# Performance work log

Hardware: AMD Instinct MI355X
Metric: run time of the kernel (lower is better)

## Reference

```python
import jax, jax.numpy as jnp
import numpy as np

N = 200_000   # nodes
E = 6_400_000 # edges (avg degree 32)


def setup_inputs() -> dict:
    key = jax.random.key(0)
    k = jax.random.split(key, 6)
    x = jax.random.normal(k[0], (N, 2), dtype=jnp.float32)
    edge_index = jax.random.randint(k[1], (2, E), 0, N, dtype=jnp.int32)
    # GCNConv(2, 8) and GCNConv(8, 4) parameters (Glorot-ish init, zero bias as in PyG)
    W1 = jax.random.normal(k[2], (2, 8), dtype=jnp.float32) * (1.0 / np.sqrt(2.0))
    b1 = jnp.zeros((8,), dtype=jnp.float32)
    W2 = jax.random.normal(k[3], (8, 4), dtype=jnp.float32) * (1.0 / np.sqrt(8.0))
    b2 = jnp.zeros((4,), dtype=jnp.float32)
    return {"x": x, "edge_index": edge_index, "W1": W1, "b1": b1, "W2": W2, "b2": b2}


def _gcn_conv(x, src, dst, norm, W, b, n):
    # PyG GCNConv: linear transform, normalized gather/scatter-add, bias after aggregation
    h = x @ W                                   # [N, F_out]
    msg = h[src] * norm[:, None]                # gather + edge-wise scale, [E', F_out]
    agg = jax.ops.segment_sum(msg, dst, num_segments=n)  # scatter-add at targets
    return agg + b


def reference(x, edge_index, W1, b1, W2, b2):
    n = x.shape[0]
    # add self-loops (PyG default add_self_loops=True)
    loops = jnp.arange(n, dtype=edge_index.dtype)
    src = jnp.concatenate([edge_index[0], loops])
    dst = jnp.concatenate([edge_index[1], loops])
    # symmetric degree normalization: deg computed at targets with unit edge weights
    deg = jax.ops.segment_sum(jnp.ones_like(src, dtype=x.dtype), dst, num_segments=n)
    deg_inv_sqrt = jnp.where(deg > 0, jax.lax.rsqrt(jnp.maximum(deg, 1.0)), 0.0)
    norm = deg_inv_sqrt[src] * deg_inv_sqrt[dst]  # [E']

    h = jax.nn.relu(_gcn_conv(x, src, dst, norm, W1, b1, n))
    out = _gcn_conv(h, src, dst, norm, W2, b2, n)
    return out
```

## Files before the change

### kernel.cpp

```cpp
#include <hip/hip_runtime.h>


#define EPB   8192
#define PART  2048
#define LPBIT 11
#define SRCB  18
#define BC    4
#define RSTR  2049
#define STCAP 17408


__global__ __launch_bounds__(512) void countA_kernel(
    const int* __restrict__ dst, int* __restrict__ cntmat, int E, int P) {
    __shared__ int cnt[128];
    int tid = threadIdx.x;
    if (tid < 128) cnt[tid] = 0;
    __syncthreads();
    int nv4 = E >> 2;
    int b4 = (blockIdx.x * EPB) >> 2;
    int e4 = min(b4 + (EPB >> 2), nv4);
    const int4* d4 = (const int4*)dst;
    #pragma unroll
    for (int k = 0; k < (EPB >> 2); k += 512) {
        int i = b4 + k + tid;
        if (i < e4) {
            int4 d = d4[i];
            atomicAdd(&cnt[d.x >> LPBIT], 1);
            atomicAdd(&cnt[d.y >> LPBIT], 1);
            atomicAdd(&cnt[d.z >> LPBIT], 1);
            atomicAdd(&cnt[d.w >> LPBIT], 1);
        }
    }
    if (blockIdx.x == gridDim.x - 1) {
        int e = (nv4 << 2) + tid;
        if (e < E) atomicAdd(&cnt[dst[e] >> LPBIT], 1);
    }
    __syncthreads();
    int* row = cntmat + (size_t)blockIdx.x * P;
    if (tid < P) row[tid] = cnt[tid];
}

__global__ __launch_bounds__(256) void colscanA_kernel(
    int* __restrict__ cntmat, int* __restrict__ colTotal, int B, int P) {
    __shared__ int sdata[256];
    int p = blockIdx.x, tid = threadIdx.x;
    int v[4];
    int s = 0;
    #pragma unroll
    for (int k = 0; k < 4; k++) {
        int b = tid * 4 + k;
        v[k] = (b < B) ? cntmat[(size_t)b * P + p] : 0;
        s += v[k];
    }
    int x = s;
    sdata[tid] = x;
    __syncthreads();
    for (int off = 1; off < 256; off <<= 1) {
        int t = (tid >= off) ? sdata[tid - off] : 0;
        __syncthreads();
        x += t;
        sdata[tid] = x;
        __syncthreads();
    }
    int run = x - s;
    #pragma unroll
    for (int k = 0; k < 4; k++) {
        int b = tid * 4 + k;
        if (b < B) cntmat[(size_t)b * P + p] = run;
        run += v[k];
    }
    if (tid == 255) colTotal[p] = x;
}

__global__ __launch_bounds__(256) void totalscanA_kernel(
    const int* __restrict__ colTotal, int* __restrict__ colStart,
    int P, int E) {
    __shared__ int sdata[256];
    int tid = threadIdx.x;
    int v[4];
    int s = 0;
    #pragma unroll
    for (int k = 0; k < 4; k++) {
        int i = tid * 4 + k;
        v[k] = (i < P) ? colTotal[i] : 0;
        s += v[k];
    }
    int x = s;
    sdata[tid] = x;
    __syncthreads();
    for (int off = 1; off < 256; off <<= 1) {
        int t = (tid >= off) ? sdata[tid - off] : 0;
        __syncthreads();
        x += t;
        sdata[tid] = x;
        __syncthreads();
    }
    int run = x - s;
    #pragma unroll
    for (int k = 0; k < 4; k++) {
        int i = tid * 4 + k;
        if (i < P) colStart[i] = run;
        run += v[k];
    }
    if (tid == 0) colStart[P] = E;
}

__global__ __launch_bounds__(512) void scatterA_kernel(
    const int* __restrict__ src, const int* __restrict__ dst,
    const int* __restrict__ cntmat, const int* __restrict__ colStart,
    unsigned* __restrict__ packed, int E, int P) {
    __shared__ int cur[128];
    int tid = threadIdx.x;
    if (tid < P) cur[tid] = colStart[tid] + cntmat[(size_t)blockIdx.x * P + tid];
    __syncthreads();
    int nv4 = E >> 2;
    int b4 = (blockIdx.x * EPB) >> 2;
    int e4 = min(b4 + (EPB >> 2), nv4);
    const int4* d4 = (const int4*)dst;
    const int4* s4 = (const int4*)src;
    #pragma unroll
    for (int k = 0; k < (EPB >> 2); k += 512) {
        int i = b4 + k + tid;
        if (i < e4) {
            int4 d = d4[i];
            int4 sv = s4[i];
            int p0 = atomicAdd(&cur[d.x >> LPBIT], 1);
            packed[p0] = ((unsigned)(d.x & (PART - 1)) << SRCB) | (unsigned)sv.x;
            int p1 = atomicAdd(&cur[d.y >> LPBIT], 1);
            packed[p1] = ((unsigned)(d.y & (PART - 1)) << SRCB) | (unsigned)sv.y;
            int p2 = atomicAdd(&cur[d.z >> LPBIT], 1);
            packed[p2] = ((unsigned)(d.z & (PART - 1)) << SRCB) | (unsigned)sv.z;
            int p3 = atomicAdd(&cur[d.w >> LPBIT], 1);
            packed[p3] = ((unsigned)(d.w & (PART - 1)) << SRCB) | (unsigned)sv.w;
        }
    }
    if (blockIdx.x == gridDim.x - 1) {
        int e = (nv4 << 2) + tid;
        if (e < E) {
            int d = dst[e];
            int pos = atomicAdd(&cur[d >> LPBIT], 1);
            packed[pos] = ((unsigned)(d & (PART - 1)) << SRCB) | (unsigned)src[e];
        }
    }
}


__global__ __launch_bounds__(512) void localC_kernel(
    const unsigned* __restrict__ packed, const int* __restrict__ colStart,
    int* __restrict__ runStart, int* __restrict__ srcsorted) {
    __shared__ int hist[PART];
    __shared__ int sdata[512];
    __shared__ unsigned stage[STCAP];
    int tid = threadIdx.x;
    int dp = blockIdx.x >> 2, b = blockIdx.x & (BC - 1);
    int s0 = colStart[dp], len = colStart[dp + 1] - s0;
    int lo = s0 + (int)(((long long)len * b) / BC);
    int hi = s0 + (int)(((long long)len * (b + 1)) / BC);
    for (int k = tid; k < PART; k += 512) hist[k] = 0;
    __syncthreads();
    for (int i = lo + tid; i < hi; i += 512)
        atomicAdd(&hist[packed[i] >> SRCB], 1);
    __syncthreads();
    int off = tid * 4;
    int v0 = hist[off], v1 = hist[off + 1], v2 = hist[off + 2], v3 = hist[off + 3];
    int s = v0 + v1 + v2 + v3;
    int x = s;
    sdata[tid] = x;
    __syncthreads();
    for (int o = 1; o < 512; o <<= 1) {
        int t = (tid >= o) ? sdata[tid - o] : 0;
        __syncthreads();
        x += t;
        sdata[tid] = x;
        __syncthreads();
    }
    int run = x - s;
    int* rs = runStart + (size_t)(dp * BC + b) * RSTR;
    int c0 = lo + run, c1 = c0 + v0, c2 = c1 + v1, c3 = c2 + v2;
    rs[off] = c0; rs[off + 1] = c1; rs[off + 2] = c2; rs[off + 3] = c3;
    __syncthreads();
    hist[off] = c0; hist[off + 1] = c1; hist[off + 2] = c2; hist[off + 3] = c3;
    if (tid == 0) rs[PART] = hi;
    __syncthreads();
    int total = hi - lo;
    bool ovf = total > STCAP;
    for (int i = lo + tid; i < hi; i += 512) {
        unsigned w = packed[i];
        int pos = atomicAdd(&hist[w >> SRCB], 1);
        unsigned sv = w & ((1u << SRCB) - 1);
        if (!ovf) stage[pos - lo] = sv;
        else srcsorted[pos] = sv;
    }
    __syncthreads();
    if (!ovf)
        for (int j = tid; j < total; j += 512) srcsorted[lo + j] = (int)stage[j];
}


__global__ __launch_bounds__(512) void dinvg_kernel(
    const int* __restrict__ runStart, const float* __restrict__ x,
    float* __restrict__ dinv, float* __restrict__ g, int n) {
    int i = blockIdx.x * 512 + threadIdx.x;
    if (i >= n) return;
    int dp = i >> LPBIT, ld = i & (PART - 1);
    int deg = 0;
    #pragma unroll
    for (int b = 0; b < BC; b++) {
        const int* rs = runStart + (size_t)(dp * BC + b) * RSTR + ld;
        deg += rs[1] - rs[0];
    }
    float d = rsqrtf((float)deg + 1.0f);
    dinv[i] = d;
    float2 xv = ((const float2*)x)[i];
    ((float2*)g)[i] = make_float2(xv.x * d, xv.y * d);
}

__global__ __launch_bounds__(512) void agg1_kernel(
    const int* __restrict__ runStart, const int* __restrict__ srcsorted,
    const float* __restrict__ g, const float* __restrict__ dinv,
    const float* __restrict__ W1, const float* __restrict__ b1,
    const float* __restrict__ W2, float* __restrict__ hs2, int n) {
    int i = blockIdx.x * 512 + threadIdx.x;
    if (i >= n) return;
    int dp = i >> LPBIT, ld = i & (PART - 1);
    const float2* gp = (const float2*)g;
    float s0 = 0.0f, s1 = 0.0f;
    #pragma unroll
    for (int b = 0; b < BC; b++) {
        const int* rs = runStart + (size_t)(dp * BC + b) * RSTR + ld;
        int p0 = rs[0], p1 = rs[1];
        int p = p0;
        for (; p + 4 <= p1; p += 4) {
            int a = srcsorted[p], bb = srcsorted[p + 1];
            int c = srcsorted[p + 2], e = srcsorted[p + 3];
            float2 w0 = gp[a], w1 = gp[bb], w2 = gp[c], w3 = gp[e];
            s0 += w0.x + w1.x + w2.x + w3.x;
            s1 += w0.y + w1.y + w2.y + w3.y;
        }
        for (; p < p1; p++) {
            float2 w = gp[srcsorted[p]];
            s0 += w.x;
            s1 += w.y;
        }
    }
    float d = dinv[i];
    float2 gi = gp[i];
    s0 = (s0 + gi.x) * d;
    s1 = (s1 + gi.y) * d;
    float h[8];
    #pragma unroll
    for (int f = 0; f < 8; f++)
        h[f] = fmaxf(s0 * W1[f] + s1 * W1[8 + f] + b1[f], 0.0f);
    float oc[4];
    #pragma unroll
    for (int k = 0; k < 4; k++) {
        float a = 0.0f;
        #pragma unroll
        for (int f = 0; f < 8; f++) a += h[f] * W2[4 * f + k];
        oc[k] = a * d;
    }
    float4 o;
    o.x = oc[0]; o.y = oc[1]; o.z = oc[2]; o.w = oc[3];
    *(float4*)(hs2 + 4 * (size_t)i) = o;
}

__global__ __launch_bounds__(512) void agg2_kernel(
    const int* __restrict__ runStart, const int* __restrict__ srcsorted,
    const float* __restrict__ hs2, const float* __restrict__ dinv,
    const float* __restrict__ b2, float* __restrict__ out, int n) {
    int i = blockIdx.x * 512 + threadIdx.x;
    if (i >= n) return;
    int dp = i >> LPBIT, ld = i & (PART - 1);
    const float4* hp = (const float4*)hs2;
    float s0 = 0.0f, s1 = 0.0f, s2 = 0.0f, s3 = 0.0f;
    #pragma unroll
    for (int b = 0; b < BC; b++) {
        const int* rs = runStart + (size_t)(dp * BC + b) * RSTR + ld;
        int p0 = rs[0], p1 = rs[1];
        int p = p0;
        for (; p + 4 <= p1; p += 4) {
            int a = srcsorted[p], bb = srcsorted[p + 1];
            int c = srcsorted[p + 2], e = srcsorted[p + 3];
            float4 w0 = hp[a], w1 = hp[bb], w2 = hp[c], w3 = hp[e];
            s0 += w0.x + w1.x + w2.x + w3.x;
            s1 += w0.y + w1.y + w2.y + w3.y;
            s2 += w0.z + w1.z + w2.z + w3.z;
            s3 += w0.w + w1.w + w2.w + w3.w;
        }
        for (; p < p1; p++) {
            float4 w = hp[srcsorted[p]];
            s0 += w.x; s1 += w.y; s2 += w.z; s3 += w.w;
        }
    }
    float d = dinv[i];
    float4 hi2 = hp[i];
    float4 o;
    o.x = d * (s0 + hi2.x) + b2[0];
    o.y = d * (s1 + hi2.y) + b2[1];
    o.z = d * (s2 + hi2.z) + b2[2];
    o.w = d * (s3 + hi2.w) + b2[3];
    *(float4*)(out + 4 * (size_t)i) = o;
}

extern "C" void kernel_launch(void* const* d_in, const int* in_sizes, int n_in,
                              void* d_out, int out_size, void* d_ws, size_t ws_size,
                              hipStream_t stream) {
    const float* x   = (const float*)d_in[0];
    const int*   ei  = (const int*)d_in[1];
    const float* W1  = (const float*)d_in[2];
    const float* b1  = (const float*)d_in[3];
    const float* W2  = (const float*)d_in[4];
    const float* b2  = (const float*)d_in[5];
    float* out = (float*)d_out;

    const int n = in_sizes[0] / 2;
    const int E = in_sizes[1] / 2;
    const int* src = ei;
    const int* dst = ei + E;

    const int P  = (n + PART - 1) >> LPBIT;
    const int B1 = (E + EPB - 1) / EPB;

    int* ws = (int*)d_ws;
    int* colTotal = ws;
    int* colStart = ws + 1024;
    int* cntmatA  = ws + 2048;
    size_t cmsz = (((size_t)B1 * P) + 3) & ~(size_t)3;
    int* runStart = cntmatA + cmsz;
    size_t rssz = (((size_t)P * BC * RSTR) + 3) & ~(size_t)3;
    unsigned* packed = (unsigned*)(runStart + rssz);
    int* srcsorted = (int*)(packed + E);
    size_t nd = (size_t)P << LPBIT;
    float* dinv = (float*)packed;
    float* g    = dinv + nd;
    float* hs2  = g + 2 * nd;

    const int gN = (n + 511) / 512;

    countA_kernel    <<<B1, 512, 0, stream>>>(dst, cntmatA, E, P);
    colscanA_kernel  <<<P, 256, 0, stream>>>(cntmatA, colTotal, B1, P);
    totalscanA_kernel<<<1, 256, 0, stream>>>(colTotal, colStart, P, E);
    scatterA_kernel  <<<B1, 512, 0, stream>>>(src, dst, cntmatA, colStart, packed, E, P);
    localC_kernel    <<<P * BC, 512, 0, stream>>>(packed, colStart, runStart, srcsorted);
    dinvg_kernel     <<<gN, 512, 0, stream>>>(runStart, x, dinv, g, n);
    agg1_kernel      <<<gN, 512, 0, stream>>>(runStart, srcsorted, g, dinv, W1, b1, W2, hs2, n);
    agg2_kernel      <<<gN, 512, 0, stream>>>(runStart, srcsorted, hs2, dinv, b2, out, n);
}
```

Measured before the change: 247.6 us.

## Stage gathered neighbor features in LDS and aggregate with per-slice partials

Each aggregation layer is split into a partial kernel and a combine kernel. In the partial kernel, a block owns a slice of destination nodes within one bucket, cooperatively gathers all neighbor feature rows into shared memory with coalesced index reads, and then sums per node per feature channel. A separate combine kernel adds the partials across the four buckets and applies the dense transforms. This is meant to replace the thread-per-node gather loops, which suffer load imbalance and divergence, at the cost of two extra launches and a partial buffer round trip through global memory.

```diff
diff --git a/kernel.cpp b/kernel.cpp
--- a/kernel.cpp
+++ b/kernel.cpp
@@ -8,6 +8,10 @@
 #define BC    4
 #define RSTR  2049
 #define STCAP 17408
+#define NSL1  256
+#define CAP1  2304
+#define NSL2  128
+#define CAP2  1280
 
 
 __global__ __launch_bounds__(512) void countA_kernel(
@@ -189,7 +193,7 @@
         int pos = atomicAdd(&hist[w >> SRCB], 1);
         unsigned sv = w & ((1u << SRCB) - 1);
         if (!ovf) stage[pos - lo] = sv;
-        else srcsorted[pos] = sv;
+        else srcsorted[pos] = (int)sv;
     }
     __syncthreads();
     if (!ovf)
@@ -215,91 +219,130 @@
     ((float2*)g)[i] = make_float2(xv.x * d, xv.y * d);
 }
 
-__global__ __launch_bounds__(512) void agg1_kernel(
-    const int* __restrict__ runStart, const int* __restrict__ srcsorted,
-    const float* __restrict__ g, const float* __restrict__ dinv,
-    const float* __restrict__ W1, const float* __restrict__ b1,
-    const float* __restrict__ W2, float* __restrict__ hs2, int n) {
+
+__global__ __launch_bounds__(512) void agg1p_kernel(
+    const int* __restrict__ srcsorted, const int* __restrict__ runStart,
+    const float* __restrict__ g, float* __restrict__ partial1) {
+    __shared__ float2 stage[CAP1];
+    __shared__ int srs[NSL1 + 1];
+    int tid = threadIdx.x;
+    int bid = blockIdx.x;
+    int sl = bid & 7, rb = bid >> 3;
+    const int* rs = runStart + (size_t)rb * RSTR + sl * NSL1;
+    if (tid <= NSL1) srs[tid] = rs[tid];
+    __syncthreads();
+    int lo = srs[0], hi = srs[NSL1];
+    const float2* gp = (const float2*)g;
+    bool ovf = (hi - lo) > CAP1;
+    if (!ovf)
+        for (int e = lo + tid; e < hi; e += 512)
+            stage[e - lo] = gp[srcsorted[e]];
+    __syncthreads();
+    int nid = tid >> 1, c = tid & 1;
+    int a = srs[nid] - lo, bnd = srs[nid + 1] - lo;
+    float acc = 0.0f;
+    if (!ovf) {
+        const float* st = (const float*)stage;
+        for (int j = a; j < bnd; j++) acc += st[j * 2 + c];
+    } else {
+        for (int j = a; j < bnd; j++)
+            acc += g[2 * (size_t)srcsorted[lo + j] + c];
+    }
+    partial1[(size_t)bid * 512 + tid] = acc;
+}
+
+__global__ __launch_bounds__(512) void combine1_kernel(
+    const float* __restrict__ partial1, const float* __restrict__ g,
+    const float* __restrict__ dinv, const float* __restrict__ W1,
+    const float* __restrict__ b1, const float* __restrict__ W2,
+    float* __restrict__ hs2, int n) {
     int i = blockIdx.x * 512 + threadIdx.x;
     if (i >= n) return;
     int dp = i >> LPBIT, ld = i & (PART - 1);
-    const float2* gp = (const float2*)g;
+    int sl = ld >> 8, off = ld & (NSL1 - 1);
     float s0 = 0.0f, s1 = 0.0f;
     #pragma unroll
     for (int b = 0; b < BC; b++) {
-        const int* rs = runStart + (size_t)(dp * BC + b) * RSTR + ld;
-        int p0 = rs[0], p1 = rs[1];
-        int p = p0;
-        for (; p + 4 <= p1; p += 4) {
-            int a = srcsorted[p], bb = srcsorted[p + 1];
-            int c = srcsorted[p + 2], e = srcsorted[p + 3];
-            float2 w0 = gp[a], w1 = gp[bb], w2 = gp[c], w3 = gp[e];
-            s0 += w0.x + w1.x + w2.x + w3.x;
-            s1 += w0.y + w1.y + w2.y + w3.y;
-        }
-        for (; p < p1; p++) {
-            float2 w = gp[srcsorted[p]];
-            s0 += w.x;
-            s1 += w.y;
-        }
+        int bid = ((dp * BC + b) << 3) | sl;
+        const float* q = partial1 + (size_t)bid * 512 + off * 2;
+        s0 += q[0];
+        s1 += q[1];
     }
     float d = dinv[i];
-    float2 gi = gp[i];
+    float2 gi = ((const float2*)g)[i];
     s0 = (s0 + gi.x) * d;
     s1 = (s1 + gi.y) * d;
-    float h[8];
-    #pragma unroll
-    for (int f = 0; f < 8; f++)
-        h[f] = fmaxf(s0 * W1[f] + s1 * W1[8 + f] + b1[f], 0.0f);
-    float oc[4];
-    #pragma unroll
-    for (int k = 0; k < 4; k++) {
-        float a = 0.0f;
-        #pragma unroll
-        for (int f = 0; f < 8; f++) a += h[f] * W2[4 * f + k];
-        oc[k] = a * d;
+    float oc0 = 0.0f, oc1 = 0.0f, oc2 = 0.0f, oc3 = 0.0f;
+    #pragma unroll
+    for (int f = 0; f < 8; f++) {
+        float h = fmaxf(s0 * W1[f] + s1 * W1[8 + f] + b1[f], 0.0f);
+        oc0 += h * W2[4 * f];
+        oc1 += h * W2[4 * f + 1];
+        oc2 += h * W2[4 * f + 2];
+        oc3 += h * W2[4 * f + 3];
     }
     float4 o;
-    o.x = oc[0]; o.y = oc[1]; o.z = oc[2]; o.w = oc[3];
-    *(float4*)(hs2 + 4 * (size_t)i) = o;
-}
-
-__global__ __launch_bounds__(512) void agg2_kernel(
-    const int* __restrict__ runStart, const int* __restrict__ srcsorted,
-    const float* __restrict__ hs2, const float* __restrict__ dinv,
-    const float* __restrict__ b2, float* __restrict__ out, int n) {
+    o.x = oc0 * d; o.y = oc1 * d; o.z = oc2 * d; o.w = oc3 * d;
+    ((float4*)hs2)[i] = o;
+}
+
+__global__ __launch_bounds__(512) void agg2p_kernel(
+    const int* __restrict__ srcsorted, const int* __restrict__ runStart,
+    const float* __restrict__ hs2, float* __restrict__ partial2) {
+    __shared__ float4 stage[CAP2];
+    __shared__ int srs[NSL2 + 1];
+    int tid = threadIdx.x;
+    int bid = blockIdx.x;
+    int sl = bid & 15, rb = bid >> 4;
+    const int* rs = runStart + (size_t)rb * RSTR + sl * NSL2;
+    if (tid <= NSL2) srs[tid] = rs[tid];
+    __syncthreads();
+    int lo = srs[0], hi = srs[NSL2];
+    const float4* hp = (const float4*)hs2;
+    bool ovf = (hi - lo) > CAP2;
+    if (!ovf)
+        for (int e = lo + tid; e < hi; e += 512)
+            stage[e - lo] = hp[srcsorted[e]];
+    __syncthreads();
+    int nid = tid >> 2, c = tid & 3;
+    int a = srs[nid] - lo, bnd = srs[nid + 1] - lo;
+    float acc = 0.0f;
+    if (!ovf) {
+        const float* st = (const float*)stage;
+        for (int j = a; j < bnd; j++) acc += st[j * 4 + c];
+    } else {
+        for (int j = a; j < bnd; j++)
+            acc += hs2[4 * (size_t)srcsorted[lo + j] + c];
+    }
+    partial2[(size_t)bid * 512 + tid] = acc;
+}
+
+__global__ __launch_bounds__(512) void combine2_kernel(
+    const float* __restrict__ partial2, const float* __restrict__ hs2,
+    const float* __restrict__ dinv, const float* __restrict__ b2,
+    float* __restrict__ out, int n) {
     int i = blockIdx.x * 512 + threadIdx.x;
     if (i >= n) return;
     int dp = i >> LPBIT, ld = i & (PART - 1);
-    const float4* hp = (const float4*)hs2;
+    int sl = ld >> 7, off = ld & (NSL2 - 1);
     float s0 = 0.0f, s1 = 0.0f, s2 = 0.0f, s3 = 0.0f;
     #pragma unroll
     for (int b = 0; b < BC; b++) {
-        const int* rs = runStart + (size_t)(dp * BC + b) * RSTR + ld;
-        int p0 = rs[0], p1 = rs[1];
-        int p = p0;
-        for (; p + 4 <= p1; p += 4) {
-            int a = srcsorted[p], bb = srcsorted[p + 1];
-            int c = srcsorted[p + 2], e = srcsorted[p + 3];
-            float4 w0 = hp[a], w1 = hp[bb], w2 = hp[c], w3 = hp[e];
-            s0 += w0.x + w1.x + w2.x + w3.x;
-            s1 += w0.y + w1.y + w2.y + w3.y;
-            s2 += w0.z + w1.z + w2.z + w3.z;
-            s3 += w0.w + w1.w + w2.w + w3.w;
-        }
-        for (; p < p1; p++) {
-            float4 w = hp[srcsorted[p]];
-            s0 += w.x; s1 += w.y; s2 += w.z; s3 += w.w;
-        }
+        int bid = ((dp * BC + b) << 4) | sl;
+        const float* q = partial2 + (size_t)bid * 512 + off * 4;
+        s0 += q[0];
+        s1 += q[1];
+        s2 += q[2];
+        s3 += q[3];
     }
     float d = dinv[i];
-    float4 hi2 = hp[i];
+    float4 hv = ((const float4*)hs2)[i];
     float4 o;
-    o.x = d * (s0 + hi2.x) + b2[0];
-    o.y = d * (s1 + hi2.y) + b2[1];
-    o.z = d * (s2 + hi2.z) + b2[2];
-    o.w = d * (s3 + hi2.w) + b2[3];
-    *(float4*)(out + 4 * (size_t)i) = o;
+    o.x = d * (s0 + hv.x) + b2[0];
+    o.y = d * (s1 + hv.y) + b2[1];
+    o.z = d * (s2 + hv.z) + b2[2];
+    o.w = d * (s3 + hv.w) + b2[3];
+    ((float4*)out)[i] = o;
 }
 
 extern "C" void kernel_launch(void* const* d_in, const int* in_sizes, int n_in,
@@ -334,8 +377,11 @@
     float* dinv = (float*)packed;
     float* g    = dinv + nd;
     float* hs2  = g + 2 * nd;
-
-    const int gN = (n + 511) / 512;
+    float* partial = hs2 + 4 * nd;
+
+    const int gN  = (n + 511) / 512;
+    const int gA1 = P * BC * (PART / NSL1);
+    const int gA2 = P * BC * (PART / NSL2);
 
     countA_kernel    <<<B1, 512, 0, stream>>>(dst, cntmatA, E, P);
     colscanA_kernel  <<<P, 256, 0, stream>>>(cntmatA, colTotal, B1, P);
@@ -343,6 +389,8 @@
     scatterA_kernel  <<<B1, 512, 0, stream>>>(src, dst, cntmatA, colStart, packed, E, P);
     localC_kernel    <<<P * BC, 512, 0, stream>>>(packed, colStart, runStart, srcsorted);
     dinvg_kernel     <<<gN, 512, 0, stream>>>(runStart, x, dinv, g, n);
-    agg1_kernel      <<<gN, 512, 0, stream>>>(runStart, srcsorted, g, dinv, W1, b1, W2, hs2, n);
-    agg2_kernel      <<<gN, 512, 0, stream>>>(runStart, srcsorted, hs2, dinv, b2, out, n);
-}
+    agg1p_kernel     <<<gA1, 512, 0, stream>>>(srcsorted, runStart, g, partial);
+    combine1_kernel  <<<gN, 512, 0, stream>>>(partial, g, dinv, W1, b1, W2, hs2, n);
+    agg2p_kernel     <<<gA2, 512, 0, stream>>>(srcsorted, runStart, hs2, partial);
+    combine2_kernel  <<<gN, 512, 0, stream>>>(partial, hs2, dinv, b2, out, n);
+}
```

Measured after the change: 244.6 us. Within noise of the previous version (-1.2%).
